# Optimization experiments

Measured on AMD Instinct MI355X. Metric: run time of the kernel, lower is better.

Reference implementation:

```python
import jax, jax.numpy as jnp
import numpy as np

BITS = 8
KQA_TOPK_PROP = 0.25
NUM_HEADS = 16


def quantize_pc(t, n_bits=BITS):
    # per-channel fake quantization over the last dim (torch quantize with
    # quantization_type='per_channel')
    q_max = 2 ** (n_bits - 1) - 1
    scales = jnp.max(jnp.abs(t), axis=-1, keepdims=True)
    scales = jnp.maximum(scales, 1e-5) / q_max
    return jnp.clip(jnp.round(t / scales), -q_max - 1, q_max) * scales


def setup_inputs() -> dict:
    key = jax.random.key(0)
    ks = jax.random.split(key, 5)
    B, N, C = 4, 1024, 1024
    x = jax.random.normal(ks[0], (B, N, C), dtype=jnp.float32)
    W_qkv = jax.random.normal(ks[1], (3 * C, C), dtype=jnp.float32) * (C ** -0.5)
    b_qkv = jax.random.normal(ks[2], (3 * C,), dtype=jnp.float32) * 0.02
    W_proj = jax.random.normal(ks[3], (C, C), dtype=jnp.float32) * (C ** -0.5)
    b_proj = jax.random.normal(ks[4], (C,), dtype=jnp.float32) * 0.02
    return {"x": x, "W_qkv": W_qkv, "b_qkv": b_qkv, "W_proj": W_proj, "b_proj": b_proj}


def _split_qkv(lin, B, N, H, hd):
    # [B,N,3C] -> (3,B,H,N,hd)
    t = jnp.transpose(lin.reshape(B, N, 3, H, hd), (2, 0, 3, 1, 4))
    return t[0], t[1], t[2]


def reference(x, W_qkv, b_qkv, W_proj, b_proj):
    B, N, C = x.shape
    H = NUM_HEADS
    hd = C // H
    scale = hd ** -0.5

    # --- quantized QKV path (KeyQueryAttention) ---
    q_x = quantize_pc(x)
    q_w = quantize_pc(W_qkv)
    q_b = quantize_pc(b_qkv)
    q_lin = quantize_pc(jnp.einsum('bnc,oc->bno', q_x, q_w) + q_b)
    q_q, q_k, _ = _split_qkv(q_lin, B, N, H, hd)
    q_attn = jnp.einsum('bhnd,bhmd->bhnm', q_q, q_k) * scale

    # --- topk-sliced partial-matmul approximation path ---
    r1 = int(C * KQA_TOPK_PROP) + 1  # channel slice of x / W_qkv
    topk_lin = jnp.einsum('bnc,oc->bno', x[:, :, :r1], W_qkv[:, :r1]) + b_qkv
    topk_q, topk_k, _ = _split_qkv(topk_lin, B, N, H, hd)
    r2 = int(hd * KQA_TOPK_PROP) + 1  # slices the SEQUENCE dim (dim 2), as in the torch code
    topk_attn = jnp.einsum('bhnd,bhmd->bhnm', topk_q[:, :, :r2], topk_k[:, :, :r2]) * scale

    # --- exact attention path (used for the output) ---
    lin = jnp.einsum('bnc,oc->bno', x, W_qkv) + b_qkv
    q, k, v = _split_qkv(lin, B, N, H, hd)
    attn = jax.nn.softmax(jnp.einsum('bhnd,bhmd->bhnm', q, k) * scale, axis=-1)
    out = jnp.einsum('bhnm,bhmd->bhnd', attn, v)  # [B,H,N,hd]
    out = jnp.transpose(out, (0, 2, 1, 3)).reshape(B, N, C)
    out = jnp.einsum('bnc,oc->bno', out, W_proj) + b_proj
    return out, q_attn, topk_attn
```

## Files before the change

kernel.cpp:

```cpp
#include <hip/hip_runtime.h>
#include <stdint.h>

typedef __bf16 bf16x8 __attribute__((ext_vector_type(8)));
typedef float f32x4 __attribute__((ext_vector_type(4)));
typedef int i32x4 __attribute__((ext_vector_type(4)));
typedef unsigned short u16;

#define DEVI static __device__ __forceinline__

DEVI u16 bfu(float f){
  unsigned u = __builtin_bit_cast(unsigned, f);
  unsigned r = u + 0x7fffu + ((u >> 16) & 1u);
  return (u16)(r >> 16);
}
DEVI float ubf(u16 h){
  unsigned u = ((unsigned)h) << 16;
  return __builtin_bit_cast(float, u);
}
DEVI unsigned packbf(float a, float b){
  return (unsigned)bfu(a) | ((unsigned)bfu(b) << 16);
}

DEVI void gload16(const void* g, void* s){
  __builtin_amdgcn_global_load_lds(
      (const __attribute__((address_space(1))) unsigned int*)g,
      (__attribute__((address_space(3))) unsigned int*)s, 16, 0, 0);
}

DEVI float blockReduceMax(float v, float* sred){
  for (int off = 32; off; off >>= 1) v = fmaxf(v, __shfl_xor(v, off));
  int w = threadIdx.x >> 6;
  if ((threadIdx.x & 63) == 0) sred[w] = v;
  __syncthreads();
  float r = fmaxf(fmaxf(sred[0], sred[1]), fmaxf(sred[2], sred[3]));
  __syncthreads();
  return r;
}

DEVI void quant_row_body(const float* __restrict__ in, int8_t* __restrict__ qo,
                         u16* __restrict__ bo, float* __restrict__ so, int row, float* sred){
  const int t = threadIdx.x;
  const float4 v = *(const float4*)(in + (size_t)row * 1024 + t * 4);
  float am = fmaxf(fmaxf(fabsf(v.x), fabsf(v.y)), fmaxf(fabsf(v.z), fabsf(v.w)));
  am = blockReduceMax(am, sred);
  const float s = fmaxf(am, 1e-5f) / 127.0f;
  if (t == 0) so[row] = s;
  char4 q;
  q.x = (int8_t)(int)fminf(fmaxf(rintf(v.x / s), -128.f), 127.f);
  q.y = (int8_t)(int)fminf(fmaxf(rintf(v.y / s), -128.f), 127.f);
  q.z = (int8_t)(int)fminf(fmaxf(rintf(v.z / s), -128.f), 127.f);
  q.w = (int8_t)(int)fminf(fmaxf(rintf(v.w / s), -128.f), 127.f);
  *(char4*)(qo + (size_t)row * 1024 + t * 4) = q;
  ushort4 h; h.x = bfu(v.x); h.y = bfu(v.y); h.z = bfu(v.z); h.w = bfu(v.w);
  *(ushort4*)(bo + (size_t)row * 1024 + t * 4) = h;
}

DEVI void quant_b_body(const float* __restrict__ b, float* __restrict__ qb, float* sred){
  const int t = threadIdx.x;
  float am = 0.f;
  for (int i = t; i < 3072; i += 256) am = fmaxf(am, fabsf(b[i]));
  am = blockReduceMax(am, sred);
  const float s = fmaxf(am, 1e-5f) / 127.0f;
  for (int i = t; i < 3072; i += 256){
    float q = fminf(fmaxf(rintf(b[i] / s), -128.f), 127.f);
    qb[i] = q * s;
  }
}

DEVI void topk_lin_body(int idx, const float* __restrict__ x, const float* __restrict__ Wq,
                        const float* __restrict__ bq, float* __restrict__ tlin){
  const int o = idx & 2047, bn = idx >> 11;
  const int b_ = bn / 17, n = bn % 17;
  const float* xr = x + ((size_t)b_ * 1024 + n) * 1024;
  const float* wr = Wq + (size_t)o * 1024;
  const float4* x4 = (const float4*)xr;
  const float4* w4 = (const float4*)wr;
  float s = 0.f;
  for (int c = 0; c < 64; c++){
    float4 a = x4[c], b = w4[c];
    s += a.x * b.x + a.y * b.y + a.z * b.z + a.w * b.w;
  }
  s += xr[256] * wr[256];
  tlin[idx] = s + bq[o];
}

DEVI void gemm_i8_body(char* smem, int tid, const int8_t* __restrict__ A, const int8_t* __restrict__ Bm,
    const float* __restrict__ sx, const float* __restrict__ sw, const float* __restrict__ qb,
    u16* __restrict__ out){
  int8_t* As = (int8_t*)smem;
  int8_t* Bs = (int8_t*)(smem + 8192);
  const int t = threadIdx.x, l = t & 63, w = t >> 6;
  const int m0 = (tid / 24) * 128, n0 = (tid % 24) * 128;
  const int wm = (w >> 1) * 64, wn = (w & 1) * 64, lr = l & 15, lg = l >> 4;
  i32x4 acc[4][4];
  i32x4 z = {0, 0, 0, 0};
  for (int i = 0; i < 4; i++) for (int j = 0; j < 4; j++) acc[i][j] = z;
  for (int kt = 0; kt < 16; kt++){
    __syncthreads();
    for (int it = 0; it < 2; it++){
      int c = w * 2 + it;
      int idx = c * 64 + l;
      int r = idx >> 2, boff = (idx & 3) * 16;
      gload16(A  + (size_t)(m0 + r) * 1024 + kt * 64 + boff, &As[c * 1024]);
      gload16(Bm + (size_t)(n0 + r) * 1024 + kt * 64 + boff, &Bs[c * 1024]);
    }
    __syncthreads();
    i32x4 a[4], b[4];
    for (int i = 0; i < 4; i++) a[i] = *(const i32x4*)(&As[(wm + i * 16 + lr) * 64 + lg * 16]);
    for (int j = 0; j < 4; j++) b[j] = *(const i32x4*)(&Bs[(wn + j * 16 + lr) * 64 + lg * 16]);
    for (int i = 0; i < 4; i++)
      for (int j = 0; j < 4; j++)
        acc[i][j] = __builtin_amdgcn_mfma_i32_16x16x64_i8(a[i], b[j], acc[i][j], 0, 0, 0);
  }
  for (int i = 0; i < 4; i++){
    int row = m0 + wm + i * 16 + lg * 4;
    for (int j = 0; j < 4; j++){
      int col = n0 + wn + j * 16 + lr;
      float swc = sw[col], qbc = qb[col];
      for (int r = 0; r < 4; r++)
        out[(size_t)(row + r) * 3072 + col] = bfu((float)acc[i][j][r] * sx[row + r] * swc + qbc);
    }
  }
}

template<int MODE>
DEVI void gemm_bf16_body(char* smem, int tid, const u16* __restrict__ A, const u16* __restrict__ Bm,
    const float* __restrict__ bias, void* __restrict__ outp, int K, int N, int nxb){
  u16* As = (u16*)smem;
  u16* Bs = (u16*)(smem + 8192);
  const int t = threadIdx.x, l = t & 63, w = t >> 6;
  const int m0 = (tid / nxb) * 128, n0 = (tid % nxb) * 128;
  const int wm = (w >> 1) * 64, wn = (w & 1) * 64, lr = l & 15, lg = l >> 4;
  f32x4 acc[4][4];
  f32x4 z = {0.f, 0.f, 0.f, 0.f};
  for (int i = 0; i < 4; i++) for (int j = 0; j < 4; j++) acc[i][j] = z;
  const int nkt = K >> 5;
  for (int kt = 0; kt < nkt; kt++){
    __syncthreads();
    for (int it = 0; it < 2; it++){
      int c = w * 2 + it;
      int idx = c * 64 + l;
      int r = idx >> 2, off = (idx & 3) * 8;
      gload16(A  + (size_t)(m0 + r) * K + kt * 32 + off, &As[c * 512]);
      gload16(Bm + (size_t)(n0 + r) * K + kt * 32 + off, &Bs[c * 512]);
    }
    __syncthreads();
    bf16x8 a[4], b[4];
    for (int i = 0; i < 4; i++) a[i] = *(const bf16x8*)(&As[(wm + i * 16 + lr) * 32 + lg * 8]);
    for (int j = 0; j < 4; j++) b[j] = *(const bf16x8*)(&Bs[(wn + j * 16 + lr) * 32 + lg * 8]);
    for (int i = 0; i < 4; i++)
      for (int j = 0; j < 4; j++)
        acc[i][j] = __builtin_amdgcn_mfma_f32_16x16x32_bf16(a[i], b[j], acc[i][j], 0, 0, 0);
  }
  for (int i = 0; i < 4; i++){
    int row = m0 + wm + i * 16 + lg * 4;
    for (int j = 0; j < 4; j++){
      int col = n0 + wn + j * 16 + lr;
      float bc = bias[col];
      for (int r = 0; r < 4; r++){
        float v = acc[i][j][r] + bc;
        if (MODE == 0){
          int s = col >> 10, h = (col >> 6) & 15, d = col & 63;
          int b_ = (row + r) >> 10, n = (row + r) & 1023;
          ((u16*)outp)[(((size_t)(s * 64 + b_ * 16 + h)) * 1024 + n) * 64 + d] = bfu(v);
        } else {
          ((float*)outp)[(size_t)(row + r) * N + col] = v;
        }
      }
    }
  }
}

DEVI void topk_attn_body(int b2, const float* __restrict__ tlin, float* __restrict__ outp){
  const int idx = b2 * 256 + threadIdx.x;
  if (idx >= 4 * 16 * 17 * 17) return;
  const int mm = idx % 17; int rest = idx / 17;
  const int nn = rest % 17; rest /= 17;
  const int h = rest % 16; const int b_ = rest / 16;
  const float* tq = tlin + ((size_t)(b_ * 17 + nn)) * 2048 + h * 64;
  const float* tk = tlin + ((size_t)(b_ * 17 + mm)) * 2048 + 1024 + h * 64;
  float s = 0.f;
  for (int d = 0; d < 64; d++) s += tq[d] * tk[d];
  outp[71303168 + idx] = s * 0.125f;
}

DEVI void qlin_quant_body(float* sred, int row, const u16* __restrict__ qlin,
                          float* __restrict__ s_ql, int8_t* __restrict__ iq, int8_t* __restrict__ ik){
  const int t = threadIdx.x;
  const u16* rp = qlin + (size_t)row * 3072;
  float am = 0.f;
  for (int i = 0; i < 3; i++){
    ushort4 v = *(const ushort4*)(rp + t * 4 + i * 1024);
    am = fmaxf(am, fmaxf(fmaxf(fabsf(ubf(v.x)), fabsf(ubf(v.y))),
                         fmaxf(fabsf(ubf(v.z)), fabsf(ubf(v.w)))));
  }
  am = blockReduceMax(am, sred);
  const float s = fmaxf(am, 1e-5f) / 127.0f;
  if (t == 0) s_ql[row] = s;
  const int b_ = row >> 10, n = row & 1023;
  const int o0 = t * 8;
  int8_t* dst = (o0 < 1024) ? iq : ik;
  const int oo = o0 & 1023, h = oo >> 6, d = oo & 63;
  const size_t base = (((size_t)(b_ * 16 + h) * 1024 + n) * 64 + d);
  ushort4 v0 = *(const ushort4*)(rp + o0);
  ushort4 v1 = *(const ushort4*)(rp + o0 + 4);
  union { int8_t c[8]; unsigned long long u; } pk;
  pk.c[0] = (int8_t)(int)fminf(fmaxf(rintf(ubf(v0.x) / s), -128.f), 127.f);
  pk.c[1] = (int8_t)(int)fminf(fmaxf(rintf(ubf(v0.y) / s), -128.f), 127.f);
  pk.c[2] = (int8_t)(int)fminf(fmaxf(rintf(ubf(v0.z) / s), -128.f), 127.f);
  pk.c[3] = (int8_t)(int)fminf(fmaxf(rintf(ubf(v0.w) / s), -128.f), 127.f);
  pk.c[4] = (int8_t)(int)fminf(fmaxf(rintf(ubf(v1.x) / s), -128.f), 127.f);
  pk.c[5] = (int8_t)(int)fminf(fmaxf(rintf(ubf(v1.y) / s), -128.f), 127.f);
  pk.c[6] = (int8_t)(int)fminf(fmaxf(rintf(ubf(v1.z) / s), -128.f), 127.f);
  pk.c[7] = (int8_t)(int)fminf(fmaxf(rintf(ubf(v1.w) / s), -128.f), 127.f);
  *(unsigned long long*)(dst + base) = pk.u;
}

DEVI void attn_body(u16* vt, int qt, int bz, const u16* __restrict__ qkv, u16* __restrict__ aout){
  const int t = threadIdx.x, l = t & 63, w = t >> 6, lr = l & 15, lg = l >> 4;
  const int b_ = bz >> 4, h = bz & 15;
  const u16* Q  = qkv + (size_t)bz * 65536;
  const u16* Kg = qkv + (size_t)(64 + bz) * 65536;
  const u16* Vg = qkv + (size_t)(128 + bz) * 65536;
  const int q0 = qt * 64 + w * 16;
  const bf16x8 bq0 = *(const bf16x8*)(Q + (size_t)(q0 + lr) * 64 + lg * 8);
  const bf16x8 bq1 = *(const bf16x8*)(Q + (size_t)(q0 + lr) * 64 + 32 + lg * 8);
  float m = -1e30f, lsum = 0.f;
  f32x4 o[4];
  f32x4 zf = {0.f, 0.f, 0.f, 0.f};
  for (int dt = 0; dt < 4; dt++) o[dt] = zf;
  const int hi = lg & 1, tt = lg >> 1;
  const int srcA = lr + 32 * hi, srcB = srcA + 16;
  const int vr = t >> 3, voff = (t & 7) * 8;
  {
    uint4 vv = *(const uint4*)(Vg + (size_t)vr * 64 + voff);
    const u16* pv = (const u16*)&vv;
    for (int j = 0; j < 8; j++) vt[(0 * 64 + voff + j) * 40 + vr] = pv[j];
  }
  __syncthreads();
  int cur = 0;
  for (int kv0 = 0; kv0 < 1024; kv0 += 32){
    const bf16x8 ak00 = *(const bf16x8*)(Kg + (size_t)(kv0 + lr) * 64 + lg * 8);
    const bf16x8 ak01 = *(const bf16x8*)(Kg + (size_t)(kv0 + lr) * 64 + 32 + lg * 8);
    const bf16x8 ak10 = *(const bf16x8*)(Kg + (size_t)(kv0 + 16 + lr) * 64 + lg * 8);
    const bf16x8 ak11 = *(const bf16x8*)(Kg + (size_t)(kv0 + 16 + lr) * 64 + 32 + lg * 8);
    const bool more = (kv0 + 32) < 1024;
    uint4 vn = {0, 0, 0, 0};
    if (more) vn = *(const uint4*)(Vg + (size_t)(kv0 + 32 + vr) * 64 + voff);
    f32x4 st[2];
    {
      f32x4 c = zf;
      c = __builtin_amdgcn_mfma_f32_16x16x32_bf16(ak00, bq0, c, 0, 0, 0);
      c = __builtin_amdgcn_mfma_f32_16x16x32_bf16(ak01, bq1, c, 0, 0, 0);
      st[0] = c;
      c = zf;
      c = __builtin_amdgcn_mfma_f32_16x16x32_bf16(ak10, bq0, c, 0, 0, 0);
      c = __builtin_amdgcn_mfma_f32_16x16x32_bf16(ak11, bq1, c, 0, 0, 0);
      st[1] = c;
    }
    float tmax = -1e30f;
    for (int kvt = 0; kvt < 2; kvt++)
      for (int r = 0; r < 4; r++){ st[kvt][r] *= 0.125f; tmax = fmaxf(tmax, st[kvt][r]); }
    tmax = fmaxf(tmax, __shfl_xor(tmax, 16));
    tmax = fmaxf(tmax, __shfl_xor(tmax, 32));
    const float mn = fmaxf(m, tmax);
    const float f = __expf(m - mn);
    m = mn;
    float p[2][4], psum = 0.f;
    for (int kvt = 0; kvt < 2; kvt++)
      for (int r = 0; r < 4; r++){ float e = __expf(st[kvt][r] - mn); p[kvt][r] = e; psum += e; }
    psum += __shfl_xor(psum, 16);
    psum += __shfl_xor(psum, 32);
    lsum = lsum * f + psum;
    for (int dt = 0; dt < 4; dt++) for (int r = 0; r < 4; r++) o[dt][r] *= f;
    int pk00 = (int)packbf(p[0][0], p[0][1]), pk01 = (int)packbf(p[0][2], p[0][3]);
    int pk10 = (int)packbf(p[1][0], p[1][1]), pk11 = (int)packbf(p[1][2], p[1][3]);
    int a0 = __shfl(pk00, srcA), a1 = __shfl(pk10, srcA);
    int b0 = __shfl(pk01, srcA), b1 = __shfl(pk11, srcA);
    int c0 = __shfl(pk00, srcB), c1 = __shfl(pk10, srcB);
    int d0 = __shfl(pk01, srcB), d1 = __shfl(pk11, srcB);
    union { unsigned u[4]; bf16x8 v; } bp;
    bp.u[0] = (unsigned)(tt ? a1 : a0);
    bp.u[1] = (unsigned)(tt ? b1 : b0);
    bp.u[2] = (unsigned)(tt ? c1 : c0);
    bp.u[3] = (unsigned)(tt ? d1 : d0);
    for (int dt = 0; dt < 4; dt++){
      bf16x8 av = *(const bf16x8*)(&vt[(cur * 64 + dt * 16 + lr) * 40 + lg * 8]);
      o[dt] = __builtin_amdgcn_mfma_f32_16x16x32_bf16(av, bp.v, o[dt], 0, 0, 0);
    }
    if (more){
      const u16* pv = (const u16*)&vn;
      for (int j = 0; j < 8; j++) vt[((cur ^ 1) * 64 + voff + j) * 40 + vr] = pv[j];
    }
    __syncthreads();
    cur ^= 1;
  }
  const float rn = 1.0f / lsum;
  for (int dt = 0; dt < 4; dt++){
    ushort4 hv;
    hv.x = bfu(o[dt][0] * rn); hv.y = bfu(o[dt][1] * rn);
    hv.z = bfu(o[dt][2] * rn); hv.w = bfu(o[dt][3] * rn);
    *(ushort4*)(aout + ((size_t)(b_ * 1024 + q0 + lr)) * 1024 + h * 64 + dt * 16 + lg * 4) = hv;
  }
}

DEVI void qattn_body(int b2, const int8_t* __restrict__ iq, const int8_t* __restrict__ ik,
    const float* __restrict__ s_ql, float* __restrict__ outp){
  const int t = threadIdx.x, l = t & 63, w = t >> 6, lr = l & 15, lg = l >> 4;
  const int n0 = (b2 & 7) * 128, m0 = ((b2 >> 3) & 7) * 128, bz = b2 >> 6;
  const int wm = (w >> 1) * 64, wn = (w & 1) * 64;
  const int b_ = bz >> 4;
  const int8_t* Aq = iq + (size_t)bz * 65536;
  const int8_t* Bk = ik + (size_t)bz * 65536;
  i32x4 a[4], b[4];
  for (int i = 0; i < 4; i++) a[i] = *(const i32x4*)(Aq + (size_t)(m0 + wm + i * 16 + lr) * 64 + lg * 16);
  for (int j = 0; j < 4; j++) b[j] = *(const i32x4*)(Bk + (size_t)(n0 + wn + j * 16 + lr) * 64 + lg * 16);
  float* op = outp + 4194304 + (size_t)bz * 1048576;
  i32x4 z = {0, 0, 0, 0};
  for (int i = 0; i < 4; i++){
    int row = m0 + wm + i * 16 + lg * 4;
    for (int j = 0; j < 4; j++){
      i32x4 acc = __builtin_amdgcn_mfma_i32_16x16x64_i8(a[i], b[j], z, 0, 0, 0);
      int col = n0 + wn + j * 16 + lr;
      float sc = s_ql[b_ * 1024 + col] * 0.125f;
      for (int r = 0; r < 4; r++)
        op[(size_t)(row + r) * 1024 + col] = (float)acc[r] * s_ql[b_ * 1024 + row + r] * sc;
    }
  }
}

__global__ __launch_bounds__(256) void stageA(
    const float* __restrict__ x, const float* __restrict__ Wq, const float* __restrict__ bq,
    const float* __restrict__ Wp,
    int8_t* __restrict__ ix, u16* __restrict__ xb, float* __restrict__ sx,
    int8_t* __restrict__ iw, u16* __restrict__ wb, float* __restrict__ sw,
    float* __restrict__ qbv, u16* __restrict__ Wpb, float* __restrict__ tlin){
  __shared__ float sred[4];
  const int bid = blockIdx.x, t = threadIdx.x;
  if (bid < 4096){
    quant_row_body(x, ix, xb, sx, bid, sred);
  } else if (bid < 7168){
    quant_row_body(Wq, iw, wb, sw, bid - 4096, sred);
  } else if (bid == 7168){
    quant_b_body(bq, qbv, sred);
  } else if (bid < 7169 + 1024){
    const int i = ((bid - 7169) * 256 + t) * 4;
    float4 v = *(const float4*)(Wp + i);
    ushort4 h; h.x = bfu(v.x); h.y = bfu(v.y); h.z = bfu(v.z); h.w = bfu(v.w);
    *(ushort4*)(Wpb + i) = h;
  } else {
    topk_lin_body((bid - 8193) * 256 + t, x, Wq, bq, tlin);
  }
}

__global__ __launch_bounds__(256) void stageB(
    const int8_t* __restrict__ ix, const int8_t* __restrict__ iw, const float* __restrict__ sx,
    const float* __restrict__ sw, const float* __restrict__ qbv, u16* __restrict__ qlin,
    const u16* __restrict__ xb, const u16* __restrict__ wb, const float* __restrict__ bq,
    u16* __restrict__ qkv, const float* __restrict__ tlin, float* __restrict__ dout){
  __shared__ __align__(16) char smem[16384];
  const int bid = blockIdx.x;
  if (bid < 768){
    const int tid = (bid & 7) * 96 + (bid >> 3);
    gemm_i8_body(smem, tid, ix, iw, sx, sw, qbv, qlin);
  } else if (bid < 1536){
    const int g = bid - 768;
    const int tid = (g & 7) * 96 + (g >> 3);
    gemm_bf16_body<0>(smem, tid, xb, wb, bq, qkv, 1024, 3072, 24);
  } else topk_attn_body(bid - 1536, tlin, dout);
}

__global__ __launch_bounds__(256) void stageC(
    const u16* __restrict__ qkv, u16* __restrict__ aout,
    const u16* __restrict__ qlin, float* __restrict__ sql,
    int8_t* __restrict__ iq, int8_t* __restrict__ ik){
  __shared__ __align__(16) char smem[10240];
  const int bid = blockIdx.x;
  if (bid < 1024){
    const int wk = (bid & 7) * 128 + (bid >> 3);
    attn_body((u16*)smem, wk & 15, wk >> 4, qkv, aout);
  }
  else qlin_quant_body((float*)smem, bid - 1024, qlin, sql, iq, ik);
}

__global__ __launch_bounds__(256) void stageD(
    const u16* __restrict__ aout, const u16* __restrict__ Wpb, const float* __restrict__ bp,
    float* __restrict__ dout,
    const int8_t* __restrict__ iq, const int8_t* __restrict__ ik, const float* __restrict__ sql){
  __shared__ __align__(16) char smem[16384];
  const int bid = blockIdx.x;
  if (bid < 256) gemm_bf16_body<1>(smem, bid, aout, Wpb, bp, dout, 1024, 1024, 8);
  else {
    const int g = bid - 256;
    const int w = (g & 7) * 512 + (g >> 3);
    qattn_body(w, iq, ik, sql, dout);
  }
}

extern "C" void kernel_launch(void* const* d_in, const int* in_sizes, int n_in,
                              void* d_out, int out_size, void* d_ws, size_t ws_size,
                              hipStream_t stream){
  const float* x  = (const float*)d_in[0];
  const float* Wq = (const float*)d_in[1];
  const float* bq = (const float*)d_in[2];
  const float* Wp = (const float*)d_in[3];
  const float* bp = (const float*)d_in[4];
  char* ws = (char*)d_ws;
  size_t off = 0;
  auto alloc = [&](size_t bytes) -> void* {
    void* p = ws + off; off += (bytes + 255) & ~(size_t)255; return p;
  };
  u16*    qlin = (u16*)   alloc(4096ull * 3072 * 2);
  int8_t* ix   = (int8_t*)alloc(4096ull * 1024);
  int8_t* iw   = (int8_t*)alloc(3072ull * 1024);
  int8_t* iq   = (int8_t*)alloc(64ull * 1024 * 64);
  int8_t* ik   = (int8_t*)alloc(64ull * 1024 * 64);
  u16*    xb   = (u16*)   alloc(4096ull * 1024 * 2);
  u16*    Wb   = (u16*)   alloc(3072ull * 1024 * 2);
  u16*    qkv  = (u16*)   alloc(3ull * 64 * 1024 * 64 * 2);
  u16*    aout = (u16*)   alloc(4096ull * 1024 * 2);
  u16*    Wpb  = (u16*)   alloc(1024ull * 1024 * 2);
  float*  tlin = (float*) alloc(4ull * 17 * 2048 * 4);
  float*  sx   = (float*) alloc(4096 * 4);
  float*  sw   = (float*) alloc(3072 * 4);
  float*  qbv  = (float*) alloc(3072 * 4);
  float*  sql  = (float*) alloc(4096 * 4);
  float*  dout = (float*)d_out;

  stageA<<<8737, 256, 0, stream>>>(x, Wq, bq, Wp, ix, xb, sx, iw, Wb, sw, qbv, Wpb, tlin);
  stageB<<<1609, 256, 0, stream>>>(ix, iw, sx, sw, qbv, qlin, xb, Wb, bq, qkv, tlin, dout);
  stageC<<<5120, 256, 0, stream>>>(qkv, aout, qlin, sql, iq, ik);
  stageD<<<4352, 256, 0, stream>>>(aout, Wpb, bp, dout, iq, ik, sql);
}
```

Measured before the change: 272.8 us.

## Use wave-per-row quantization, MFMA priority hints, and rebalance stage block assignments

```diff
diff --git a/kernel.cpp b/kernel.cpp
--- a/kernel.cpp
+++ b/kernel.cpp
@@ -25,6 +25,11 @@
   __builtin_amdgcn_global_load_lds(
       (const __attribute__((address_space(1))) unsigned int*)g,
       (__attribute__((address_space(3))) unsigned int*)s, 16, 0, 0);
+}
+
+DEVI float waveReduceMax(float v){
+  for (int off = 1; off < 64; off <<= 1) v = fmaxf(v, __shfl_xor(v, off));
+  return v;
 }
 
 DEVI float blockReduceMax(float v, float* sred){
@@ -37,22 +42,30 @@
   return r;
 }
 
-DEVI void quant_row_body(const float* __restrict__ in, int8_t* __restrict__ qo,
-                         u16* __restrict__ bo, float* __restrict__ so, int row, float* sred){
-  const int t = threadIdx.x;
-  const float4 v = *(const float4*)(in + (size_t)row * 1024 + t * 4);
-  float am = fmaxf(fmaxf(fabsf(v.x), fabsf(v.y)), fmaxf(fabsf(v.z), fabsf(v.w)));
-  am = blockReduceMax(am, sred);
+DEVI void quant_row_wave(const float* __restrict__ in, int8_t* __restrict__ qo,
+                         u16* __restrict__ bo, float* __restrict__ so, int row){
+  const int lane = threadIdx.x & 63;
+  const float* rp = in + (size_t)row * 1024;
+  float4 v[4];
+  float am = 0.f;
+  for (int i = 0; i < 4; i++){
+    v[i] = *(const float4*)(rp + i * 256 + lane * 4);
+    am = fmaxf(am, fmaxf(fmaxf(fabsf(v[i].x), fabsf(v[i].y)),
+                         fmaxf(fabsf(v[i].z), fabsf(v[i].w))));
+  }
+  am = waveReduceMax(am);
   const float s = fmaxf(am, 1e-5f) / 127.0f;
-  if (t == 0) so[row] = s;
-  char4 q;
-  q.x = (int8_t)(int)fminf(fmaxf(rintf(v.x / s), -128.f), 127.f);
-  q.y = (int8_t)(int)fminf(fmaxf(rintf(v.y / s), -128.f), 127.f);
-  q.z = (int8_t)(int)fminf(fmaxf(rintf(v.z / s), -128.f), 127.f);
-  q.w = (int8_t)(int)fminf(fmaxf(rintf(v.w / s), -128.f), 127.f);
-  *(char4*)(qo + (size_t)row * 1024 + t * 4) = q;
-  ushort4 h; h.x = bfu(v.x); h.y = bfu(v.y); h.z = bfu(v.z); h.w = bfu(v.w);
-  *(ushort4*)(bo + (size_t)row * 1024 + t * 4) = h;
+  if (lane == 0) so[row] = s;
+  for (int i = 0; i < 4; i++){
+    char4 q;
+    q.x = (int8_t)(int)fminf(fmaxf(rintf(v[i].x / s), -128.f), 127.f);
+    q.y = (int8_t)(int)fminf(fmaxf(rintf(v[i].y / s), -128.f), 127.f);
+    q.z = (int8_t)(int)fminf(fmaxf(rintf(v[i].z / s), -128.f), 127.f);
+    q.w = (int8_t)(int)fminf(fmaxf(rintf(v[i].w / s), -128.f), 127.f);
+    *(char4*)(qo + (size_t)row * 1024 + i * 256 + lane * 4) = q;
+    ushort4 h; h.x = bfu(v[i].x); h.y = bfu(v[i].y); h.z = bfu(v[i].z); h.w = bfu(v[i].w);
+    *(ushort4*)(bo + (size_t)row * 1024 + i * 256 + lane * 4) = h;
+  }
 }
 
 DEVI void quant_b_body(const float* __restrict__ b, float* __restrict__ qb, float* sred){
@@ -108,9 +121,11 @@
     i32x4 a[4], b[4];
     for (int i = 0; i < 4; i++) a[i] = *(const i32x4*)(&As[(wm + i * 16 + lr) * 64 + lg * 16]);
     for (int j = 0; j < 4; j++) b[j] = *(const i32x4*)(&Bs[(wn + j * 16 + lr) * 64 + lg * 16]);
+    __builtin_amdgcn_s_setprio(1);
     for (int i = 0; i < 4; i++)
       for (int j = 0; j < 4; j++)
         acc[i][j] = __builtin_amdgcn_mfma_i32_16x16x64_i8(a[i], b[j], acc[i][j], 0, 0, 0);
+    __builtin_amdgcn_s_setprio(0);
   }
   for (int i = 0; i < 4; i++){
     int row = m0 + wm + i * 16 + lg * 4;
@@ -148,9 +163,11 @@
     bf16x8 a[4], b[4];
     for (int i = 0; i < 4; i++) a[i] = *(const bf16x8*)(&As[(wm + i * 16 + lr) * 32 + lg * 8]);
     for (int j = 0; j < 4; j++) b[j] = *(const bf16x8*)(&Bs[(wn + j * 16 + lr) * 32 + lg * 8]);
+    __builtin_amdgcn_s_setprio(1);
     for (int i = 0; i < 4; i++)
       for (int j = 0; j < 4; j++)
         acc[i][j] = __builtin_amdgcn_mfma_f32_16x16x32_bf16(a[i], b[j], acc[i][j], 0, 0, 0);
+    __builtin_amdgcn_s_setprio(0);
   }
   for (int i = 0; i < 4; i++){
     int row = m0 + wm + i * 16 + lg * 4;
@@ -184,36 +201,32 @@
   outp[71303168 + idx] = s * 0.125f;
 }
 
-DEVI void qlin_quant_body(float* sred, int row, const u16* __restrict__ qlin,
+DEVI void qlin_quant_wave(int row, const u16* __restrict__ qlin,
                           float* __restrict__ s_ql, int8_t* __restrict__ iq, int8_t* __restrict__ ik){
-  const int t = threadIdx.x;
+  const int lane = threadIdx.x & 63;
   const u16* rp = qlin + (size_t)row * 3072;
+  uint4 raw[6];
   float am = 0.f;
-  for (int i = 0; i < 3; i++){
-    ushort4 v = *(const ushort4*)(rp + t * 4 + i * 1024);
-    am = fmaxf(am, fmaxf(fmaxf(fabsf(ubf(v.x)), fabsf(ubf(v.y))),
-                         fmaxf(fabsf(ubf(v.z)), fabsf(ubf(v.w)))));
-  }
-  am = blockReduceMax(am, sred);
+  for (int i = 0; i < 6; i++){
+    raw[i] = *(const uint4*)(rp + i * 512 + lane * 8);
+    const u16* pp = (const u16*)&raw[i];
+    for (int j = 0; j < 8; j++) am = fmaxf(am, fabsf(ubf(pp[j])));
+  }
+  am = waveReduceMax(am);
   const float s = fmaxf(am, 1e-5f) / 127.0f;
-  if (t == 0) s_ql[row] = s;
+  if (lane == 0) s_ql[row] = s;
   const int b_ = row >> 10, n = row & 1023;
-  const int o0 = t * 8;
-  int8_t* dst = (o0 < 1024) ? iq : ik;
-  const int oo = o0 & 1023, h = oo >> 6, d = oo & 63;
-  const size_t base = (((size_t)(b_ * 16 + h) * 1024 + n) * 64 + d);
-  ushort4 v0 = *(const ushort4*)(rp + o0);
-  ushort4 v1 = *(const ushort4*)(rp + o0 + 4);
-  union { int8_t c[8]; unsigned long long u; } pk;
-  pk.c[0] = (int8_t)(int)fminf(fmaxf(rintf(ubf(v0.x) / s), -128.f), 127.f);
-  pk.c[1] = (int8_t)(int)fminf(fmaxf(rintf(ubf(v0.y) / s), -128.f), 127.f);
-  pk.c[2] = (int8_t)(int)fminf(fmaxf(rintf(ubf(v0.z) / s), -128.f), 127.f);
-  pk.c[3] = (int8_t)(int)fminf(fmaxf(rintf(ubf(v0.w) / s), -128.f), 127.f);
-  pk.c[4] = (int8_t)(int)fminf(fmaxf(rintf(ubf(v1.x) / s), -128.f), 127.f);
-  pk.c[5] = (int8_t)(int)fminf(fmaxf(rintf(ubf(v1.y) / s), -128.f), 127.f);
-  pk.c[6] = (int8_t)(int)fminf(fmaxf(rintf(ubf(v1.z) / s), -128.f), 127.f);
-  pk.c[7] = (int8_t)(int)fminf(fmaxf(rintf(ubf(v1.w) / s), -128.f), 127.f);
-  *(unsigned long long*)(dst + base) = pk.u;
+  for (int i = 0; i < 4; i++){
+    const int o0 = i * 512 + lane * 8;
+    int8_t* dst = (o0 < 1024) ? iq : ik;
+    const int oo = o0 & 1023, h = oo >> 6, d = oo & 63;
+    const size_t base = (((size_t)(b_ * 16 + h) * 1024 + n) * 64 + d);
+    const u16* pp = (const u16*)&raw[i];
+    union { int8_t c[8]; unsigned long long u; } pk;
+    for (int j = 0; j < 8; j++)
+      pk.c[j] = (int8_t)(int)fminf(fmaxf(rintf(ubf(pp[j]) / s), -128.f), 127.f);
+    *(unsigned long long*)(dst + base) = pk.u;
+  }
 }
 
 DEVI void attn_body(u16* vt, int qt, int bz, const u16* __restrict__ qkv, u16* __restrict__ aout){
@@ -249,6 +262,7 @@
     if (more) vn = *(const uint4*)(Vg + (size_t)(kv0 + 32 + vr) * 64 + voff);
     f32x4 st[2];
     {
+      __builtin_amdgcn_s_setprio(1);
       f32x4 c = zf;
       c = __builtin_amdgcn_mfma_f32_16x16x32_bf16(ak00, bq0, c, 0, 0, 0);
       c = __builtin_amdgcn_mfma_f32_16x16x32_bf16(ak01, bq1, c, 0, 0, 0);
@@ -257,6 +271,7 @@
       c = __builtin_amdgcn_mfma_f32_16x16x32_bf16(ak10, bq0, c, 0, 0, 0);
       c = __builtin_amdgcn_mfma_f32_16x16x32_bf16(ak11, bq1, c, 0, 0, 0);
       st[1] = c;
+      __builtin_amdgcn_s_setprio(0);
     }
     float tmax = -1e30f;
     for (int kvt = 0; kvt < 2; kvt++)
@@ -284,10 +299,12 @@
     bp.u[1] = (unsigned)(tt ? b1 : b0);
     bp.u[2] = (unsigned)(tt ? c1 : c0);
     bp.u[3] = (unsigned)(tt ? d1 : d0);
+    __builtin_amdgcn_s_setprio(1);
     for (int dt = 0; dt < 4; dt++){
       bf16x8 av = *(const bf16x8*)(&vt[(cur * 64 + dt * 16 + lr) * 40 + lg * 8]);
       o[dt] = __builtin_amdgcn_mfma_f32_16x16x32_bf16(av, bp.v, o[dt], 0, 0, 0);
     }
+    __builtin_amdgcn_s_setprio(0);
     if (more){
       const u16* pv = (const u16*)&vn;
       for (int j = 0; j < 8; j++) vt[((cur ^ 1) * 64 + voff + j) * 40 + vr] = pv[j];
@@ -336,20 +353,23 @@
     int8_t* __restrict__ iw, u16* __restrict__ wb, float* __restrict__ sw,
     float* __restrict__ qbv, u16* __restrict__ Wpb, float* __restrict__ tlin){
   __shared__ float sred[4];
-  const int bid = blockIdx.x, t = threadIdx.x;
-  if (bid < 4096){
-    quant_row_body(x, ix, xb, sx, bid, sred);
-  } else if (bid < 7168){
-    quant_row_body(Wq, iw, wb, sw, bid - 4096, sred);
-  } else if (bid == 7168){
+  const int bid = blockIdx.x, t = threadIdx.x, wv = t >> 6;
+  if (bid < 544){
+    topk_lin_body(bid * 256 + t, x, Wq, bq, tlin);
+  } else if (bid < 1568){
+    quant_row_wave(x, ix, xb, sx, (bid - 544) * 4 + wv);
+  } else if (bid < 2336){
+    quant_row_wave(Wq, iw, wb, sw, (bid - 1568) * 4 + wv);
+  } else if (bid < 2848){
+    const int i = ((bid - 2336) * 256 + t) * 8;
+    float4 a = *(const float4*)(Wp + i);
+    float4 b = *(const float4*)(Wp + i + 4);
+    ushort4 h0; h0.x = bfu(a.x); h0.y = bfu(a.y); h0.z = bfu(a.z); h0.w = bfu(a.w);
+    ushort4 h1; h1.x = bfu(b.x); h1.y = bfu(b.y); h1.z = bfu(b.z); h1.w = bfu(b.w);
+    *(ushort4*)(Wpb + i) = h0;
+    *(ushort4*)(Wpb + i + 4) = h1;
+  } else {
     quant_b_body(bq, qbv, sred);
-  } else if (bid < 7169 + 1024){
-    const int i = ((bid - 7169) * 256 + t) * 4;
-    float4 v = *(const float4*)(Wp + i);
-    ushort4 h; h.x = bfu(v.x); h.y = bfu(v.y); h.z = bfu(v.z); h.w = bfu(v.w);
-    *(ushort4*)(Wpb + i) = h;
-  } else {
-    topk_lin_body((bid - 8193) * 256 + t, x, Wq, bq, tlin);
   }
 }
 
@@ -357,30 +377,34 @@
     const int8_t* __restrict__ ix, const int8_t* __restrict__ iw, const float* __restrict__ sx,
     const float* __restrict__ sw, const float* __restrict__ qbv, u16* __restrict__ qlin,
     const u16* __restrict__ xb, const u16* __restrict__ wb, const float* __restrict__ bq,
-    u16* __restrict__ qkv, const float* __restrict__ tlin, float* __restrict__ dout){
+    u16* __restrict__ qkv){
   __shared__ __align__(16) char smem[16384];
   const int bid = blockIdx.x;
   if (bid < 768){
     const int tid = (bid & 7) * 96 + (bid >> 3);
-    gemm_i8_body(smem, tid, ix, iw, sx, sw, qbv, qlin);
-  } else if (bid < 1536){
+    gemm_bf16_body<0>(smem, tid, xb, wb, bq, qkv, 1024, 3072, 24);
+  } else {
     const int g = bid - 768;
     const int tid = (g & 7) * 96 + (g >> 3);
-    gemm_bf16_body<0>(smem, tid, xb, wb, bq, qkv, 1024, 3072, 24);
-  } else topk_attn_body(bid - 1536, tlin, dout);
+    gemm_i8_body(smem, tid, ix, iw, sx, sw, qbv, qlin);
+  }
 }
 
 __global__ __launch_bounds__(256) void stageC(
     const u16* __restrict__ qkv, u16* __restrict__ aout,
     const u16* __restrict__ qlin, float* __restrict__ sql,
-    int8_t* __restrict__ iq, int8_t* __restrict__ ik){
+    int8_t* __restrict__ iq, int8_t* __restrict__ ik,
+    const float* __restrict__ tlin, float* __restrict__ dout){
   __shared__ __align__(16) char smem[10240];
-  const int bid = blockIdx.x;
+  const int bid = blockIdx.x, wv = threadIdx.x >> 6;
   if (bid < 1024){
     const int wk = (bid & 7) * 128 + (bid >> 3);
     attn_body((u16*)smem, wk & 15, wk >> 4, qkv, aout);
-  }
-  else qlin_quant_body((float*)smem, bid - 1024, qlin, sql, iq, ik);
+  } else if (bid < 2048){
+    qlin_quant_wave((bid - 1024) * 4 + wv, qlin, sql, iq, ik);
+  } else {
+    topk_attn_body(bid - 2048, tlin, dout);
+  }
 }
 
 __global__ __launch_bounds__(256) void stageD(
@@ -427,8 +451,8 @@
   float*  sql  = (float*) alloc(4096 * 4);
   float*  dout = (float*)d_out;
 
-  stageA<<<8737, 256, 0, stream>>>(x, Wq, bq, Wp, ix, xb, sx, iw, Wb, sw, qbv, Wpb, tlin);
-  stageB<<<1609, 256, 0, stream>>>(ix, iw, sx, sw, qbv, qlin, xb, Wb, bq, qkv, tlin, dout);
-  stageC<<<5120, 256, 0, stream>>>(qkv, aout, qlin, sql, iq, ik);
+  stageA<<<2849, 256, 0, stream>>>(x, Wq, bq, Wp, ix, xb, sx, iw, Wb, sw, qbv, Wpb, tlin);
+  stageB<<<1536, 256, 0, stream>>>(ix, iw, sx, sw, qbv, qlin, xb, Wb, bq, qkv);
+  stageC<<<2121, 256, 0, stream>>>(qkv, aout, qlin, sql, iq, ik, tlin, dout);
   stageD<<<4352, 256, 0, stream>>>(aout, Wpb, bp, dout, iq, ik, sql);
 }
```

Result: faster. 241.3 us (median of 2 runs) (-11.5%).
